# Kernel tuning notes

Measured on AMD Instinct MI355X. Metric: run time of the kernel, lower is better.

## Reference

```python
import jax, jax.numpy as jnp
from jax import lax
import numpy as np

EPS = 1e-6
DN = ('NCHW', 'OIHW', 'NCHW')  # conv dimension numbers matching torch F.conv2d


def setup_inputs() -> dict:
    key = jax.random.key(0)
    kx, ky = jax.random.split(key)
    B, C, H, W = 16, 3, 512, 512
    x = jax.random.normal(kx, (B, C, H, W), dtype=jnp.float32)
    y = jax.random.normal(ky, (B, C, H, W), dtype=jnp.float32)
    return {"x": x, "y": y}


def _box_smooth(v):
    # 7x7 uniform kernel repeated over 3 input channels -> 1 output channel,
    # every tap weighted 1/49 (matches kernel.repeat(1,3,1,1) in torch).
    k = jnp.full((1, v.shape[1], 7, 7), 1.0 / 49.0, dtype=v.dtype)
    return lax.conv_general_dilated(v, k, window_strides=(1, 1),
                                    padding=[(3, 3), (3, 3)],
                                    dimension_numbers=DN)


def reference(x, y):
    # conv is linear, so conv(x) - conv(y) == conv(x - y); avoids one conv pass
    diff = _box_smooth(x - y)           # [B, 1, H, W]
    return jnp.mean(jnp.sqrt(diff * diff + EPS))  # scalar Charbonnier loss
```

## Files before the change

kernel.cpp:

```cpp
#include <hip/hip_runtime.h>
#include <math.h>


namespace {
constexpr int kB = 16, kH = 512, kW = 512;
constexpr int NT = 256;
constexpr int ROWS = 4;
constexpr int RIN = ROWS + 6;
constexpr int NBLK = kB * kH / (ROWS * 4);
}

__global__ __launch_bounds__(NT, 2)
void charbox_kernel(const float* __restrict__ x, const float* __restrict__ y,
                    float* __restrict__ out) {
  const int tid = threadIdx.x, lane = tid & 63, wv = tid >> 6;
  const int b    = blockIdx.x >> 5;
  const int row0 = ((blockIdx.x & 31) << 4) + (wv << 2);
  const size_t HW = (size_t)kH * kW;
  const float* xb = x + (size_t)b * 3 * HW;
  const float* yb = y + (size_t)b * 3 * HW;
  const int colb = lane << 3;

  float4 buf[2][6][2];
  float ring[3][8], vsum[8];
  float acc = 0.f;
#pragma unroll
  for (int j = 0; j < 8; ++j) vsum[j] = 0.f;

  auto loadrow = [&](int h, float4 (&r)[6][2]) {
    const int hc = min(max(h, 0), kH - 1);
    const float* px = xb + (size_t)hc * kW + colb;
    const float* py = yb + (size_t)hc * kW + colb;
    r[0][0] = *(const float4*)(px);            r[0][1] = *(const float4*)(px + 4);
    r[1][0] = *(const float4*)(px + HW);       r[1][1] = *(const float4*)(px + HW + 4);
    r[2][0] = *(const float4*)(px + 2 * HW);   r[2][1] = *(const float4*)(px + 2 * HW + 4);
    r[3][0] = *(const float4*)(py);            r[3][1] = *(const float4*)(py + 4);
    r[4][0] = *(const float4*)(py + HW);       r[4][1] = *(const float4*)(py + HW + 4);
    r[5][0] = *(const float4*)(py + 2 * HW);   r[5][1] = *(const float4*)(py + 2 * HW + 4);
  };

  loadrow(row0 - 3, buf[0]);

#pragma unroll
  for (int rr = 0; rr < RIN; ++rr) {
    float4 (&cb)[6][2] = buf[rr & 1];
    if (rr + 1 < RIN) loadrow(row0 - 3 + rr + 1, buf[(rr + 1) & 1]);

    const float m = ((unsigned)(row0 - 3 + rr) < (unsigned)kH) ? 1.f : 0.f;
    float z[8];
#pragma unroll
    for (int p = 0; p < 2; ++p) {
      const float4 dx0 = cb[0][p], dx1 = cb[1][p], dx2 = cb[2][p];
      const float4 dy0 = cb[3][p], dy1 = cb[4][p], dy2 = cb[5][p];
      z[4 * p + 0] = ((dx0.x - dy0.x) + (dx1.x - dy1.x) + (dx2.x - dy2.x)) * m;
      z[4 * p + 1] = ((dx0.y - dy0.y) + (dx1.y - dy1.y) + (dx2.y - dy2.y)) * m;
      z[4 * p + 2] = ((dx0.z - dy0.z) + (dx1.z - dy1.z) + (dx2.z - dy2.z)) * m;
      z[4 * p + 3] = ((dx0.w - dy0.w) + (dx1.w - dy1.w) + (dx2.w - dy2.w)) * m;
    }

    float l5 = __shfl_up(z[5], 1, 64);
    float l6 = __shfl_up(z[6], 1, 64);
    float l7 = __shfl_up(z[7], 1, 64);
    float r0 = __shfl_down(z[0], 1, 64);
    float r1 = __shfl_down(z[1], 1, 64);
    float r2 = __shfl_down(z[2], 1, 64);
    if (lane == 0)  { l5 = 0.f; l6 = 0.f; l7 = 0.f; }
    if (lane == 63) { r0 = 0.f; r1 = 0.f; r2 = 0.f; }

    const float e[14] = {l5, l6, l7, z[0], z[1], z[2], z[3],
                         z[4], z[5], z[6], z[7], r0, r1, r2};
    float hrow[8];
    hrow[0] = ((e[0] + e[1]) + (e[2] + e[3])) + ((e[4] + e[5]) + e[6]);
#pragma unroll
    for (int c = 1; c < 8; ++c) hrow[c] = hrow[c - 1] + e[c + 6] - e[c - 1];

    if (rr < 3) {
#pragma unroll
      for (int j = 0; j < 8; ++j) { vsum[j] += hrow[j]; ring[rr][j] = hrow[j]; }
    } else if (rr < 6) {
#pragma unroll
      for (int j = 0; j < 8; ++j) vsum[j] += hrow[j];
    } else if (rr == 6) {
#pragma unroll
      for (int j = 0; j < 8; ++j) {
        vsum[j] += hrow[j];
        const float d = vsum[j] * (1.0f / 49.0f);
        acc += sqrtf(fmaf(d, d, 1e-6f));
      }
    } else {
      const int ri = (rr >= 7) ? rr - 7 : 0;
#pragma unroll
      for (int j = 0; j < 8; ++j) {
        vsum[j] += hrow[j] - ring[ri][j];
        const float d = vsum[j] * (1.0f / 49.0f);
        acc += sqrtf(fmaf(d, d, 1e-6f));
      }
    }
  }

#pragma unroll
  for (int off = 32; off > 0; off >>= 1) acc += __shfl_down(acc, off, 64);
  __shared__ float red[NT / 64];
  if (lane == 0) red[wv] = acc;
  __syncthreads();
  if (tid == 0) {
    const float ssum = red[0] + red[1] + red[2] + red[3];
    atomicAdd(out, ssum * (1.0f / ((float)kB * (float)kH * (float)kW)));
  }
}

extern "C" void kernel_launch(void* const* d_in, const int* in_sizes, int n_in,
                              void* d_out, int out_size, void* d_ws, size_t ws_size,
                              hipStream_t stream) {
  const float* x = (const float*)d_in[0];
  const float* y = (const float*)d_in[1];
  float* out = (float*)d_out;

  charbox_kernel<<<NBLK, NT, 0, stream>>>(x, y, out);
}
```

Before: 127.8 us.

## Stream input rows via global_load_lds with double-buffered LDS per wave

Replaces register float4 loads with direct global-to-LDS asynchronous loads (global_load_lds, 16 bytes per lane), double-buffering two rows per wave with explicit vmcnt waits so the next rows are in flight while the current one is reduced. Each wave now computes 8 output rows instead of 4, which lowers the 6-row halo re-read overhead, and blocks are remapped to spread adjacent rows across the grid. The ring buffer grows to 7 rows and the block shrinks to 128 threads with 48KB of LDS and launch bounds of 1, which cuts occupancy and relies on correct hand-written waitcnt counts.

```diff
diff --git a/kernel.cpp b/kernel.cpp
--- a/kernel.cpp
+++ b/kernel.cpp
@@ -4,59 +4,83 @@
 
 namespace {
 constexpr int kB = 16, kH = 512, kW = 512;
-constexpr int NT = 256;
-constexpr int ROWS = 4;
+constexpr int NT = 128;
+constexpr int WVS = NT / 64;
+constexpr int ROWS = 8;
 constexpr int RIN = ROWS + 6;
-constexpr int NBLK = kB * kH / (ROWS * 4);
+constexpr int NBLK = kB * kH / (ROWS * WVS);
 }
 
-__global__ __launch_bounds__(NT, 2)
+__device__ __forceinline__ void gload_lds16(const float* g, float* l) {
+  __builtin_amdgcn_global_load_lds(
+      (const __attribute__((address_space(1))) unsigned int*)g,
+      (__attribute__((address_space(3))) unsigned int*)l, 16, 0, 0);
+}
+
+__global__ __launch_bounds__(NT, 1)
 void charbox_kernel(const float* __restrict__ x, const float* __restrict__ y,
                     float* __restrict__ out) {
+  __shared__ float lds[WVS][2][6][kW];
+  __shared__ float red[WVS];
+
   const int tid = threadIdx.x, lane = tid & 63, wv = tid >> 6;
-  const int b    = blockIdx.x >> 5;
-  const int row0 = ((blockIdx.x & 31) << 4) + (wv << 2);
+
+  const int rb    = (blockIdx.x & 7) * (NBLK / 8) + (blockIdx.x >> 3);
+  const int b     = rb >> 5;
+  const int row0  = ((rb & 31) << 4) + wv * ROWS;
+
   const size_t HW = (size_t)kH * kW;
   const float* xb = x + (size_t)b * 3 * HW;
   const float* yb = y + (size_t)b * 3 * HW;
-  const int colb = lane << 3;
+  const float* base[6] = {xb, xb + HW, xb + 2 * HW, yb, yb + HW, yb + 2 * HW};
 
-  float4 buf[2][6][2];
-  float ring[3][8], vsum[8];
+  auto issue_row = [&](int h, int bi) {
+    const int hc = min(max(h, 0), kH - 1);
+    const size_t ro = (size_t)hc * kW;
+#pragma unroll
+    for (int s = 0; s < 6; ++s) {
+      const float* g = base[s] + ro + lane * 4;
+#pragma unroll
+      for (int c = 0; c < 2; ++c)
+        gload_lds16(g + c * 256, &lds[wv][bi][s][c * 256]);
+    }
+  };
+
+  float ring[7][8], vsum[8];
   float acc = 0.f;
 #pragma unroll
   for (int j = 0; j < 8; ++j) vsum[j] = 0.f;
 
-  auto loadrow = [&](int h, float4 (&r)[6][2]) {
-    const int hc = min(max(h, 0), kH - 1);
-    const float* px = xb + (size_t)hc * kW + colb;
-    const float* py = yb + (size_t)hc * kW + colb;
-    r[0][0] = *(const float4*)(px);            r[0][1] = *(const float4*)(px + 4);
-    r[1][0] = *(const float4*)(px + HW);       r[1][1] = *(const float4*)(px + HW + 4);
-    r[2][0] = *(const float4*)(px + 2 * HW);   r[2][1] = *(const float4*)(px + 2 * HW + 4);
-    r[3][0] = *(const float4*)(py);            r[3][1] = *(const float4*)(py + 4);
-    r[4][0] = *(const float4*)(py + HW);       r[4][1] = *(const float4*)(py + HW + 4);
-    r[5][0] = *(const float4*)(py + 2 * HW);   r[5][1] = *(const float4*)(py + 2 * HW + 4);
-  };
-
-  loadrow(row0 - 3, buf[0]);
+  issue_row(row0 - 3, 0);
+  issue_row(row0 - 2, 1);
 
 #pragma unroll
   for (int rr = 0; rr < RIN; ++rr) {
-    float4 (&cb)[6][2] = buf[rr & 1];
-    if (rr + 1 < RIN) loadrow(row0 - 3 + rr + 1, buf[(rr + 1) & 1]);
+    if (rr < RIN - 2)       asm volatile("s_waitcnt vmcnt(12)" ::: "memory");
+    else if (rr == RIN - 2) asm volatile("s_waitcnt vmcnt(0)"  ::: "memory");
 
+    const int bi = rr & 1;
     const float m = ((unsigned)(row0 - 3 + rr) < (unsigned)kH) ? 1.f : 0.f;
     float z[8];
 #pragma unroll
-    for (int p = 0; p < 2; ++p) {
-      const float4 dx0 = cb[0][p], dx1 = cb[1][p], dx2 = cb[2][p];
-      const float4 dy0 = cb[3][p], dy1 = cb[4][p], dy2 = cb[5][p];
-      z[4 * p + 0] = ((dx0.x - dy0.x) + (dx1.x - dy1.x) + (dx2.x - dy2.x)) * m;
-      z[4 * p + 1] = ((dx0.y - dy0.y) + (dx1.y - dy1.y) + (dx2.y - dy2.y)) * m;
-      z[4 * p + 2] = ((dx0.z - dy0.z) + (dx1.z - dy1.z) + (dx2.z - dy2.z)) * m;
-      z[4 * p + 3] = ((dx0.w - dy0.w) + (dx1.w - dy1.w) + (dx2.w - dy2.w)) * m;
+    for (int j = 0; j < 8; ++j) z[j] = 0.f;
+#pragma unroll
+    for (int s = 0; s < 6; ++s) {
+      const float4 p0 = *(const float4*)&lds[wv][bi][s][lane * 8];
+      const float4 p1 = *(const float4*)&lds[wv][bi][s][lane * 8 + 4];
+      if (s < 3) {
+        z[0] += p0.x; z[1] += p0.y; z[2] += p0.z; z[3] += p0.w;
+        z[4] += p1.x; z[5] += p1.y; z[6] += p1.z; z[7] += p1.w;
+      } else {
+        z[0] -= p0.x; z[1] -= p0.y; z[2] -= p0.z; z[3] -= p0.w;
+        z[4] -= p1.x; z[5] -= p1.y; z[6] -= p1.z; z[7] -= p1.w;
+      }
     }
+#pragma unroll
+    for (int j = 0; j < 8; ++j) z[j] *= m;
+
+    asm volatile("s_waitcnt lgkmcnt(0)" ::: "memory");
+    if (rr + 2 < RIN) issue_row(row0 - 3 + rr + 2, bi);
 
     float l5 = __shfl_up(z[5], 1, 64);
     float l6 = __shfl_up(z[6], 1, 64);
@@ -74,24 +98,16 @@
 #pragma unroll
     for (int c = 1; c < 8; ++c) hrow[c] = hrow[c - 1] + e[c + 6] - e[c - 1];
 
-    if (rr < 3) {
+    if (rr < 7) {
 #pragma unroll
-      for (int j = 0; j < 8; ++j) { vsum[j] += hrow[j]; ring[rr][j] = hrow[j]; }
-    } else if (rr < 6) {
+      for (int j = 0; j < 8; ++j) { ring[rr][j] = hrow[j]; vsum[j] += hrow[j]; }
+    } else {
 #pragma unroll
-      for (int j = 0; j < 8; ++j) vsum[j] += hrow[j];
-    } else if (rr == 6) {
+      for (int j = 0; j < 8; ++j) vsum[j] += hrow[j] - ring[rr - 7][j];
+    }
+    if (rr >= 6) {
 #pragma unroll
       for (int j = 0; j < 8; ++j) {
-        vsum[j] += hrow[j];
-        const float d = vsum[j] * (1.0f / 49.0f);
-        acc += sqrtf(fmaf(d, d, 1e-6f));
-      }
-    } else {
-      const int ri = (rr >= 7) ? rr - 7 : 0;
-#pragma unroll
-      for (int j = 0; j < 8; ++j) {
-        vsum[j] += hrow[j] - ring[ri][j];
         const float d = vsum[j] * (1.0f / 49.0f);
         acc += sqrtf(fmaf(d, d, 1e-6f));
       }
@@ -100,11 +116,12 @@
 
 #pragma unroll
   for (int off = 32; off > 0; off >>= 1) acc += __shfl_down(acc, off, 64);
-  __shared__ float red[NT / 64];
   if (lane == 0) red[wv] = acc;
   __syncthreads();
   if (tid == 0) {
-    const float ssum = red[0] + red[1] + red[2] + red[3];
+    float ssum = 0.f;
+#pragma unroll
+    for (int w = 0; w < WVS; ++w) ssum += red[w];
     atomicAdd(out, ssum * (1.0f / ((float)kB * (float)kH * (float)kW)));
   }
 }
```

Measured after the change: 124.4 us. 2.7% less time.

## Split into channel-difference pass and single-plane box-filter loss kernel

Applied to the files above, without the earlier changes.

Adds a first kernel that reduces x−y across the three channels into a single-plane workspace. The box-filter/Charbonnier kernel then reads that one plane instead of six. This removes the halo over-read of six input planes in the fused kernel and lightens its per-row loads. In exchange it adds an extra launch and a write and read round trip of the intermediate plane through memory.

```diff
diff --git a/kernel.cpp b/kernel.cpp
--- a/kernel.cpp
+++ b/kernel.cpp
@@ -4,71 +4,78 @@
 
 namespace {
 constexpr int kB = 16, kH = 512, kW = 512;
-constexpr int NT = 256;
+constexpr size_t HW = (size_t)kH * kW;
+constexpr int NPX4 = kB * kH * kW / 4;
+constexpr int CS4  = (int)(HW / 4);
+
+constexpr int NT2  = 256;
 constexpr int ROWS = 4;
-constexpr int RIN = ROWS + 6;
-constexpr int NBLK = kB * kH / (ROWS * 4);
+constexpr int RIN  = ROWS + 6;
+constexpr int NBLK2 = kB * kH / (ROWS * (NT2 / 64));
 }
 
-__global__ __launch_bounds__(NT, 2)
-void charbox_kernel(const float* __restrict__ x, const float* __restrict__ y,
-                    float* __restrict__ out) {
+__global__ __launch_bounds__(256)
+void zdiff_kernel(const float* __restrict__ x, const float* __restrict__ y,
+                  float* __restrict__ z) {
+  const int i = blockIdx.x * 256 + threadIdx.x;
+  const int b = i >> 16;
+  const int o = i & 65535;
+  const float4* px = (const float4*)(x + (size_t)b * 3 * HW) + o;
+  const float4* py = (const float4*)(y + (size_t)b * 3 * HW) + o;
+  const float4 a0 = px[0], a1 = px[CS4], a2 = px[2 * CS4];
+  const float4 b0 = py[0], b1 = py[CS4], b2 = py[2 * CS4];
+  float4 r;
+  r.x = (a0.x - b0.x) + (a1.x - b1.x) + (a2.x - b2.x);
+  r.y = (a0.y - b0.y) + (a1.y - b1.y) + (a2.y - b2.y);
+  r.z = (a0.z - b0.z) + (a1.z - b1.z) + (a2.z - b2.z);
+  r.w = (a0.w - b0.w) + (a1.w - b1.w) + (a2.w - b2.w);
+  ((float4*)z)[i] = r;
+}
+
+__global__ __launch_bounds__(NT2, 2)
+void boxloss_kernel(const float* __restrict__ z, float* __restrict__ out) {
   const int tid = threadIdx.x, lane = tid & 63, wv = tid >> 6;
-  const int b    = blockIdx.x >> 5;
-  const int row0 = ((blockIdx.x & 31) << 4) + (wv << 2);
-  const size_t HW = (size_t)kH * kW;
-  const float* xb = x + (size_t)b * 3 * HW;
-  const float* yb = y + (size_t)b * 3 * HW;
-  const int colb = lane << 3;
+  const int strip = blockIdx.x * (NT2 / 64) + wv;
+  const int b     = strip >> 7;
+  const int row0  = (strip & 127) * ROWS;
+  const float* zb = z + (size_t)b * HW;
+  const int colb  = lane << 3;
 
-  float4 buf[2][6][2];
+  float4 buf[2][2];
   float ring[3][8], vsum[8];
   float acc = 0.f;
 #pragma unroll
   for (int j = 0; j < 8; ++j) vsum[j] = 0.f;
 
-  auto loadrow = [&](int h, float4 (&r)[6][2]) {
+  auto loadrow = [&](int h, float4 (&r)[2]) {
     const int hc = min(max(h, 0), kH - 1);
-    const float* px = xb + (size_t)hc * kW + colb;
-    const float* py = yb + (size_t)hc * kW + colb;
-    r[0][0] = *(const float4*)(px);            r[0][1] = *(const float4*)(px + 4);
-    r[1][0] = *(const float4*)(px + HW);       r[1][1] = *(const float4*)(px + HW + 4);
-    r[2][0] = *(const float4*)(px + 2 * HW);   r[2][1] = *(const float4*)(px + 2 * HW + 4);
-    r[3][0] = *(const float4*)(py);            r[3][1] = *(const float4*)(py + 4);
-    r[4][0] = *(const float4*)(py + HW);       r[4][1] = *(const float4*)(py + HW + 4);
-    r[5][0] = *(const float4*)(py + 2 * HW);   r[5][1] = *(const float4*)(py + 2 * HW + 4);
+    const float* p = zb + (size_t)hc * kW + colb;
+    r[0] = *(const float4*)p;
+    r[1] = *(const float4*)(p + 4);
   };
 
   loadrow(row0 - 3, buf[0]);
 
 #pragma unroll
   for (int rr = 0; rr < RIN; ++rr) {
-    float4 (&cb)[6][2] = buf[rr & 1];
+    float4 (&cb)[2] = buf[rr & 1];
     if (rr + 1 < RIN) loadrow(row0 - 3 + rr + 1, buf[(rr + 1) & 1]);
 
     const float m = ((unsigned)(row0 - 3 + rr) < (unsigned)kH) ? 1.f : 0.f;
-    float z[8];
-#pragma unroll
-    for (int p = 0; p < 2; ++p) {
-      const float4 dx0 = cb[0][p], dx1 = cb[1][p], dx2 = cb[2][p];
-      const float4 dy0 = cb[3][p], dy1 = cb[4][p], dy2 = cb[5][p];
-      z[4 * p + 0] = ((dx0.x - dy0.x) + (dx1.x - dy1.x) + (dx2.x - dy2.x)) * m;
-      z[4 * p + 1] = ((dx0.y - dy0.y) + (dx1.y - dy1.y) + (dx2.y - dy2.y)) * m;
-      z[4 * p + 2] = ((dx0.z - dy0.z) + (dx1.z - dy1.z) + (dx2.z - dy2.z)) * m;
-      z[4 * p + 3] = ((dx0.w - dy0.w) + (dx1.w - dy1.w) + (dx2.w - dy2.w)) * m;
-    }
+    float zv[8] = {cb[0].x * m, cb[0].y * m, cb[0].z * m, cb[0].w * m,
+                   cb[1].x * m, cb[1].y * m, cb[1].z * m, cb[1].w * m};
 
-    float l5 = __shfl_up(z[5], 1, 64);
-    float l6 = __shfl_up(z[6], 1, 64);
-    float l7 = __shfl_up(z[7], 1, 64);
-    float r0 = __shfl_down(z[0], 1, 64);
-    float r1 = __shfl_down(z[1], 1, 64);
-    float r2 = __shfl_down(z[2], 1, 64);
+    float l5 = __shfl_up(zv[5], 1, 64);
+    float l6 = __shfl_up(zv[6], 1, 64);
+    float l7 = __shfl_up(zv[7], 1, 64);
+    float r0 = __shfl_down(zv[0], 1, 64);
+    float r1 = __shfl_down(zv[1], 1, 64);
+    float r2 = __shfl_down(zv[2], 1, 64);
     if (lane == 0)  { l5 = 0.f; l6 = 0.f; l7 = 0.f; }
     if (lane == 63) { r0 = 0.f; r1 = 0.f; r2 = 0.f; }
 
-    const float e[14] = {l5, l6, l7, z[0], z[1], z[2], z[3],
-                         z[4], z[5], z[6], z[7], r0, r1, r2};
+    const float e[14] = {l5, l6, l7, zv[0], zv[1], zv[2], zv[3],
+                         zv[4], zv[5], zv[6], zv[7], r0, r1, r2};
     float hrow[8];
     hrow[0] = ((e[0] + e[1]) + (e[2] + e[3])) + ((e[4] + e[5]) + e[6]);
 #pragma unroll
@@ -88,7 +95,7 @@
         acc += sqrtf(fmaf(d, d, 1e-6f));
       }
     } else {
-      const int ri = (rr >= 7) ? rr - 7 : 0;
+      const int ri = rr - 7;
 #pragma unroll
       for (int j = 0; j < 8; ++j) {
         vsum[j] += hrow[j] - ring[ri][j];
@@ -100,7 +107,7 @@
 
 #pragma unroll
   for (int off = 32; off > 0; off >>= 1) acc += __shfl_down(acc, off, 64);
-  __shared__ float red[NT / 64];
+  __shared__ float red[NT2 / 64];
   if (lane == 0) red[wv] = acc;
   __syncthreads();
   if (tid == 0) {
@@ -115,6 +122,8 @@
   const float* x = (const float*)d_in[0];
   const float* y = (const float*)d_in[1];
   float* out = (float*)d_out;
+  float* z = (float*)d_ws;
 
-  charbox_kernel<<<NBLK, NT, 0, stream>>>(x, y, out);
+  zdiff_kernel<<<NPX4 / 256, 256, 0, stream>>>(x, y, z);
+  boxloss_kernel<<<NBLK2, NT2, 0, stream>>>(z, out);
 }
```

After: 127.1 us. About the same (-0.6%).
